# Kernel tuning notes

Measured on AMD Instinct MI355X. Metric: run time of the kernel, lower is better.

The kernel has to match this reference:

```python
import jax, jax.numpy as jnp
import numpy as np

NUM_HEADS = 16
NUM_KV_HEADS = 4
HEAD_SIZE = 128
SCALE = 1.0 / np.sqrt(128.0).astype(np.float32)
NEG_INF = -1e30


def setup_inputs() -> dict:
    key = jax.random.key(0)
    kq, kk, kv = jax.random.split(key, 3)
    B, S = 2, 2048
    query = jax.random.normal(kq, (B, NUM_HEADS, S, HEAD_SIZE), dtype=jnp.float32)
    k = jax.random.normal(kk, (B, NUM_KV_HEADS, S, HEAD_SIZE), dtype=jnp.float32)
    v = jax.random.normal(kv, (B, NUM_KV_HEADS, S, HEAD_SIZE), dtype=jnp.float32)
    return {"query": query, "key": k, "value": v}


def _attn(query, key, value):
    # query: [B, H, S, D]; key/value: [B, Hkv, S, D]; GQA with group = H // Hkv
    B, H, S, D = query.shape
    Hkv = key.shape[1]
    G = H // Hkv
    q = query.reshape(B, Hkv, G, S, D)
    # scores: [B, Hkv, G, Sq, Sk]
    scores = jnp.einsum('bkgsd,bktd->bkgst', q, key) * jnp.float32(SCALE)
    causal = jnp.tril(jnp.ones((S, S), dtype=bool))  # [Sq, Sk]
    scores = jnp.where(causal, scores, jnp.float32(NEG_INF))
    probs = jax.nn.softmax(scores, axis=-1)
    out = jnp.einsum('bkgst,bktd->bkgsd', probs, value)  # [B, Hkv, G, S, D]
    out = out.reshape(B, H, S, D)
    # transpose(1,2).reshape -> [B, S, H*D]
    return out.transpose(0, 2, 1, 3).reshape(B, S, H * D)


def reference(query, key, value):
    return _attn(query, key, value)
```

## Files before the change

### kernel.cpp

```cpp
#include <hip/hip_runtime.h>


#define S_LEN 2048
#define DH    128
#define NH    16
#define NKVH  4
#define NB    2
#define TQ    128
#define TK    64
#define NQT   (S_LEN / TQ)
#define QSCALE 0.12752749610559243f

typedef __attribute__((ext_vector_type(8))) short short8;
typedef __attribute__((ext_vector_type(4))) float f32x4;

#if __has_builtin(__builtin_amdgcn_exp2f)
#define EX2(x) __builtin_amdgcn_exp2f(x)
#else
#define EX2(x) exp2f(x)
#endif

__device__ __forceinline__ unsigned pk2(float a, float b) {
    union { float f; unsigned u; } x, y; x.f = a; y.f = b;
    return ((x.u + 0x8000u) >> 16) | ((y.u + 0x8000u) & 0xffff0000u);
}
__device__ __forceinline__ void cp16(const void* g, void* lds) {
    __builtin_amdgcn_global_load_lds(
        (const __attribute__((address_space(1))) void*)g,
        (__attribute__((address_space(3))) void*)lds, 16, 0, 0);
}

__global__ __launch_bounds__(256, 4)
void prepack(const float* __restrict__ K, const float* __restrict__ V,
             unsigned short* __restrict__ Kb, unsigned short* __restrict__ Vt) {
    if (blockIdx.y == 0) {
        const long long flat = (long long)blockIdx.x * 2048 + threadIdx.x * 8;
        const int s = (int)(flat >> 7) & (S_LEN - 1);
        const int d0 = (int)flat & 127;
        const float* p = K + flat;
        float4 x = *(const float4*)p;
        float4 y = *(const float4*)(p + 4);
        const int cs = (d0 >> 3) ^ (s & 7);
        uint4 o;
        o.x = pk2(x.x, x.y); o.y = pk2(x.z, x.w);
        o.z = pk2(y.x, y.y); o.w = pk2(y.z, y.w);
        *(uint4*)(Kb + (flat & ~127LL) + cs * 8) = o;
    } else {
        const int x = blockIdx.x;
        const int bkvh = x >> 7, sblk = (x >> 2) & 31, q = x & 3;
        const int tid = threadIdx.x;
        __shared__ unsigned Lt[64][17];
        const float* base = V + (size_t)bkvh * S_LEN * DH + (size_t)sblk * 64 * DH + q * 32;
#pragma unroll
        for (int j = 0; j < 2; ++j) {
            const int e = tid + j * 256;
            const int s = e >> 3, c4 = e & 7;
            float4 v = *(const float4*)(base + (size_t)s * DH + c4 * 4);
            Lt[s][c4 * 2]     = pk2(v.x, v.y);
            Lt[s][c4 * 2 + 1] = pk2(v.z, v.w);
        }
        __syncthreads();
        const unsigned short* lt = (const unsigned short*)&Lt[0][0];
        const int d_loc = tid >> 3, pc = tid & 7;
        const int d = q * 32 + d_loc;
        const int c_log = pc ^ (d & 7);
        unsigned short vv[8];
#pragma unroll
        for (int j = 0; j < 8; ++j) {
            const int kp = c_log * 8 + j;
            const int kv = (kp & 3) * 16 + (kp >> 2);
            vv[j] = lt[kv * 34 + d_loc];
        }
        uint4 o;
        o.x = (unsigned)vv[0] | ((unsigned)vv[1] << 16);
        o.y = (unsigned)vv[2] | ((unsigned)vv[3] << 16);
        o.z = (unsigned)vv[4] | ((unsigned)vv[5] << 16);
        o.w = (unsigned)vv[6] | ((unsigned)vv[7] << 16);
        *(uint4*)(Vt + (size_t)bkvh * S_LEN * DH + (size_t)d * S_LEN + sblk * 64 + pc * 8) = o;
    }
}

__global__ __launch_bounds__(256, 2)
void attn_fwd(const float* __restrict__ Q,
              const unsigned short* __restrict__ Kb,
              const unsigned short* __restrict__ Vtg,
              float* __restrict__ O,
              float* __restrict__ Opart,
              float* __restrict__ Lpart) {
    const int n    = blockIdx.x;
    const int g    = n & 7;
    const int b    = g >> 2;
    const int kvh  = g & 3;
    const int kk   = n >> 3;
    const int h    = kvh * 4 + (kk & 3);
    const int pr   = kk >> 2;
    const int a    = pr & 7;
    const int role = pr >> 3;
    const int sid  = ((b * NH + h) << 3) + a;

    const int tid  = threadIdx.x;
    const int w    = tid >> 6;
    const int lane = tid & 63;
    const int quad = lane >> 4;
    const int l16  = lane & 15;
    const int swz  = l16 & 7;

    int qt0, kt00, nr0, qt1; bool two_seg;
    if (role == 0) { qt0 = a;      kt00 = 0;         nr0 = 2 * a + 2;
                     qt1 = 15 - a; two_seg = true; }
    else           { qt0 = 15 - a; kt00 = 15 - 2*a;  nr0 = 17;
                     qt1 = 0;      two_seg = false; }

    __shared__ alignas(16) unsigned short Kl[2][TK][DH];
    __shared__ alignas(16) unsigned short Vl[2][DH][TK];
    __shared__ alignas(16) unsigned short Pl[TQ][64];

    const unsigned short* kb = Kb  + ((size_t)b * NKVH + kvh) * (size_t)(S_LEN * DH);
    const unsigned short* vb = Vtg + ((size_t)b * NKVH + kvh) * (size_t)(S_LEN * DH);

    auto stage = [&](int nb_, int kt) {
        const char* ks = (const char*)(kb + (size_t)kt * TK * DH);
        char* kd = (char*)&Kl[nb_][0][0] + w * 4096;
#pragma unroll
        for (int i = 0; i < 4; ++i)
            cp16(ks + w * 4096 + i * 1024 + lane * 16, kd + i * 1024);
        const char* vs = (const char*)vb + (size_t)kt * (TK * 2);
        char* vd = (char*)&Vl[nb_][0][0] + w * 4096;
#pragma unroll
        for (int i = 0; i < 4; ++i) {
            const int row = w * 32 + i * 8 + (lane >> 3);
            cp16(vs + (size_t)row * (S_LEN * 2) + (lane & 7) * 16, vd + i * 1024);
        }
    };
    auto ktof = [&](int r) { return r < nr0 ? kt00 + r : r - nr0; };

    stage(0, ktof(0));

    int qt  = qt0;
    int wq0 = qt * TQ + w * 32;
    int ntw = 2 * qt + 1 + (w >> 1);

    short8 aq[2][4];
    auto loadQ = [&]() {
#pragma unroll
        for (int sub = 0; sub < 2; ++sub) {
            const float* qp = Q + (((size_t)b * NH + h) * S_LEN + wq0 + sub * 16 + l16) * DH;
#pragma unroll
            for (int dc = 0; dc < 4; ++dc) {
                float4 xx = *(const float4*)(qp + dc * 32 + quad * 8);
                float4 yy = *(const float4*)(qp + dc * 32 + quad * 8 + 4);
                union { unsigned u[4]; short8 s; } tq;
                tq.u[0] = pk2(xx.x * QSCALE, xx.y * QSCALE);
                tq.u[1] = pk2(xx.z * QSCALE, xx.w * QSCALE);
                tq.u[2] = pk2(yy.x * QSCALE, yy.y * QSCALE);
                tq.u[3] = pk2(yy.z * QSCALE, yy.w * QSCALE);
                aq[sub][dc] = tq.s;
            }
        }
    };
    loadQ();

    f32x4 o[2][8];
    float lsum[2][4];
#pragma unroll
    for (int sub = 0; sub < 2; ++sub) {
#pragma unroll
        for (int ch = 0; ch < 8; ++ch) o[sub][ch] = (f32x4){0.f, 0.f, 0.f, 0.f};
#pragma unroll
        for (int r = 0; r < 4; ++r) lsum[sub][r] = 0.f;
    }

    __syncthreads();

    int cur = 0;
    for (int r = 0; r < 17; ++r) {
        if (r + 1 < 17) stage(cur ^ 1, ktof(r + 1));
        const int kt = ktof(r);
        if (kt < ntw) {
            const int j0 = kt * TK;
            const bool diag = (kt == ntw - 1);
            f32x4 s[2][4];
#pragma unroll
            for (int sub = 0; sub < 2; ++sub)
#pragma unroll
                for (int k4 = 0; k4 < 4; ++k4) s[sub][k4] = (f32x4){0.f, 0.f, 0.f, 0.f};
#pragma unroll
            for (int dc = 0; dc < 4; ++dc) {
#pragma unroll
                for (int k4 = 0; k4 < 4; ++k4) {
                    short8 bk = *(const short8*)&Kl[cur][k4 * 16 + l16][((dc * 4 + quad) ^ swz) * 8];
                    s[0][k4] = __builtin_amdgcn_mfma_f32_16x16x32_bf16(aq[0][dc], bk, s[0][k4], 0, 0, 0);
                    s[1][k4] = __builtin_amdgcn_mfma_f32_16x16x32_bf16(aq[1][dc], bk, s[1][k4], 0, 0, 0);
                }
            }
#pragma unroll
            for (int sub = 0; sub < 2; ++sub) {
                const int rb = wq0 + sub * 16 + quad * 4;
#pragma unroll
                for (int rr = 0; rr < 4; ++rr) {
                    float v0 = s[sub][0][rr], v1 = s[sub][1][rr];
                    float v2 = s[sub][2][rr], v3 = s[sub][3][rr];
                    if (diag) {
                        const int row = rb + rr;
                        if (j0 + l16      > row) v0 = -1e30f;
                        if (j0 + 16 + l16 > row) v1 = -1e30f;
                        if (j0 + 32 + l16 > row) v2 = -1e30f;
                        if (j0 + 48 + l16 > row) v3 = -1e30f;
                    }
                    float p0 = EX2(v0), p1 = EX2(v1), p2 = EX2(v2), p3 = EX2(v3);
                    lsum[sub][rr] += (p0 + p1) + (p2 + p3);
                    const int prow = w * 32 + sub * 16 + quad * 4 + rr;
                    const int wcol = (l16 * 8) ^ ((prow & 7) << 4);
                    *(uint2*)((char*)&Pl[0][0] + prow * 128 + wcol) =
                        make_uint2(pk2(p0, p1), pk2(p2, p3));
                }
            }
            const int rx = (l16 & 7) << 4;
#pragma unroll
            for (int kc = 0; kc < 2; ++kc) {
                const int cb = kc * 64 + quad * 16;
                short8 ap0 = *(const short8*)((const char*)&Pl[0][0] + (w * 32 + l16) * 128 + (cb ^ rx));
                short8 ap1 = *(const short8*)((const char*)&Pl[0][0] + (w * 32 + 16 + l16) * 128 + (cb ^ rx));
#pragma unroll
                for (int ch = 0; ch < 8; ++ch) {
                    short8 bv = *(const short8*)&Vl[cur][ch * 16 + l16][((kc * 4 + quad) ^ swz) * 8];
                    o[0][ch] = __builtin_amdgcn_mfma_f32_16x16x32_bf16(ap0, bv, o[0][ch], 0, 0, 0);
                    o[1][ch] = __builtin_amdgcn_mfma_f32_16x16x32_bf16(ap1, bv, o[1][ch], 0, 0, 0);
                }
            }
        }
        __syncthreads();
        cur ^= 1;
        if (two_seg && r == nr0 - 1) {
#pragma unroll
            for (int sub = 0; sub < 2; ++sub) {
#pragma unroll
                for (int rr = 0; rr < 4; ++rr) {
                    float rs = lsum[sub][rr];
                    rs += __shfl_xor(rs, 1);
                    rs += __shfl_xor(rs, 2);
                    rs += __shfl_xor(rs, 4);
                    rs += __shfl_xor(rs, 8);
                    const float invl = 1.f / rs;
                    const int row = wq0 + sub * 16 + quad * 4 + rr;
                    float* op = O + ((size_t)b * S_LEN + row) * (NH * DH) + h * DH;
#pragma unroll
                    for (int ch = 0; ch < 8; ++ch)
                        op[ch * 16 + l16] = o[sub][ch][rr] * invl;
                }
            }
            qt = qt1; wq0 = qt * TQ + w * 32; ntw = 2 * qt + 1 + (w >> 1);
            loadQ();
#pragma unroll
            for (int sub = 0; sub < 2; ++sub) {
#pragma unroll
                for (int ch = 0; ch < 8; ++ch) o[sub][ch] = (f32x4){0.f, 0.f, 0.f, 0.f};
#pragma unroll
                for (int rr = 0; rr < 4; ++rr) lsum[sub][rr] = 0.f;
            }
        }
    }

    float* lb = Lpart + (size_t)(role * 256 + sid) * 128;
#pragma unroll
    for (int sub = 0; sub < 2; ++sub) {
#pragma unroll
        for (int rr = 0; rr < 4; ++rr) {
            float rs = lsum[sub][rr];
            rs += __shfl_xor(rs, 1);
            rs += __shfl_xor(rs, 2);
            rs += __shfl_xor(rs, 4);
            rs += __shfl_xor(rs, 8);
            const int rl = w * 32 + sub * 16 + quad * 4 + rr;
            if (l16 == 0) lb[rl] = rs;
            float* op;
            if (role == 0) {
                const int row = wq0 + sub * 16 + quad * 4 + rr;
                op = O + ((size_t)b * S_LEN + row) * (NH * DH) + h * DH;
            } else {
                op = Opart + (size_t)sid * (128 * 128) + (size_t)rl * 128;
            }
#pragma unroll
            for (int ch = 0; ch < 8; ++ch)
                op[ch * 16 + l16] = o[sub][ch][rr];
        }
    }
}

__global__ __launch_bounds__(256)
void combine(const float* __restrict__ Opart, const float* __restrict__ Lpart,
             float* __restrict__ O) {
    const int blk = blockIdx.x;
    const int sid = blk >> 2;
    const int qp  = blk & 3;
    const int bh = sid >> 3, a = sid & 7;
    const int b = bh >> 4, h = bh & 15;
    const int qt = 15 - a;
    const float* o1 = Opart + (size_t)sid * (128 * 128);
    const float* l0 = Lpart + (size_t)sid * 128;
    const float* l1 = Lpart + (size_t)(256 + sid) * 128;
    const int tid = threadIdx.x;
#pragma unroll
    for (int i = 0; i < 4; ++i) {
        const int idx = qp * 1024 + i * 256 + tid;
        const int row = idx >> 5;
        const int c4  = idx & 31;
        const float inv = 1.f / (l0[row] + l1[row]);
        float* op = O + ((size_t)b * S_LEN + qt * 128 + row) * (NH * DH) + h * DH + c4 * 4;
        const float4 x = *(const float4*)op;
        const float4 y = ((const float4*)o1)[idx];
        float4 z;
        z.x = (x.x + y.x) * inv; z.y = (x.y + y.y) * inv;
        z.z = (x.z + y.z) * inv; z.w = (x.w + y.w) * inv;
        *(float4*)op = z;
    }
}

extern "C" void kernel_launch(void* const* d_in, const int* in_sizes, int n_in,
                              void* d_out, int out_size, void* d_ws, size_t ws_size,
                              hipStream_t stream) {
    const float* Q = (const float*)d_in[0];
    const float* K = (const float*)d_in[1];
    const float* V = (const float*)d_in[2];
    float* O = (float*)d_out;
    unsigned short* Kb = (unsigned short*)d_ws;
    unsigned short* Vt = Kb + (size_t)NB * NKVH * S_LEN * DH;
    float* Opart = (float*)(Vt + (size_t)NB * NKVH * S_LEN * DH);
    float* Lpart = Opart + (size_t)256 * 128 * 128;
    dim3 pgrid(NB * NKVH * (S_LEN / 16), 2);
    prepack<<<pgrid, 256, 0, stream>>>(K, V, Kb, Vt);
    attn_fwd<<<dim3(512), 256, 0, stream>>>(Q, Kb, Vt, O, Opart, Lpart);
    combine<<<dim3(1024), 256, 0, stream>>>(Opart, Lpart, O);
}
```

Measured before the change: 149.6 us.

## Compute S transposed so P feeds PV MFMA from registers, dropping LDS round-trip

Swaps the MFMA operands for QK^T so each lane holds scores for one query row across keys. The probabilities can then be packed straight into bf16 A-operands for the PV MFMA, with no write to and read back from a shared P tile. The V-transpose preprocessing permutes the key order to match this register layout. This also cuts the row-sum reduction to two cross-quad shuffles. In exchange it relies on the permuted V layout matching the MFMA lane mapping exactly, and uses a broadcast shuffle to fetch each row sum.

Measured after the change: 146.1 us. 1.02x faster.

```diff
diff --git a/kernel.cpp b/kernel.cpp
--- a/kernel.cpp
+++ b/kernel.cpp
@@ -68,7 +68,8 @@
 #pragma unroll
         for (int j = 0; j < 8; ++j) {
             const int kp = c_log * 8 + j;
-            const int kv = (kp & 3) * 16 + (kp >> 2);
+            const int kv = ((kp >> 5) & 1) * 32 + ((kp >> 2) & 1) * 16
+                         + ((kp >> 3) & 3) * 4 + (kp & 3);
             vv[j] = lt[kv * 34 + d_loc];
         }
         uint4 o;
@@ -113,19 +114,18 @@
 
     __shared__ alignas(16) unsigned short Kl[2][TK][DH];
     __shared__ alignas(16) unsigned short Vl[2][DH][TK];
-    __shared__ alignas(16) unsigned short Pl[TQ][64];
 
     const unsigned short* kb = Kb  + ((size_t)b * NKVH + kvh) * (size_t)(S_LEN * DH);
     const unsigned short* vb = Vtg + ((size_t)b * NKVH + kvh) * (size_t)(S_LEN * DH);
 
-    auto stage = [&](int nb_, int kt) {
+    auto stage = [&](int buf, int kt) {
         const char* ks = (const char*)(kb + (size_t)kt * TK * DH);
-        char* kd = (char*)&Kl[nb_][0][0] + w * 4096;
+        char* kd = (char*)&Kl[buf][0][0] + w * 4096;
 #pragma unroll
         for (int i = 0; i < 4; ++i)
             cp16(ks + w * 4096 + i * 1024 + lane * 16, kd + i * 1024);
         const char* vs = (const char*)vb + (size_t)kt * (TK * 2);
-        char* vd = (char*)&Vl[nb_][0][0] + w * 4096;
+        char* vd = (char*)&Vl[buf][0][0] + w * 4096;
 #pragma unroll
         for (int i = 0; i < 4; ++i) {
             const int row = w * 32 + i * 8 + (lane >> 3);
@@ -136,9 +136,12 @@
 
     stage(0, ktof(0));
 
-    int qt  = qt0;
-    int wq0 = qt * TQ + w * 32;
-    int ntw = 2 * qt + 1 + (w >> 1);
+    int qt, wq0, ntw;
+    auto setseg = [&](int q) {
+        qt = q; wq0 = qt * TQ + w * 32;
+        ntw = 2 * qt + 1 + (w >> 1);
+    };
+    setseg(qt0);
 
     short8 aq[2][4];
     auto loadQ = [&]() {
@@ -161,14 +164,11 @@
     loadQ();
 
     f32x4 o[2][8];
-    float lsum[2][4];
-#pragma unroll
-    for (int sub = 0; sub < 2; ++sub) {
+    float lsum[2] = {0.f, 0.f};
+#pragma unroll
+    for (int sub = 0; sub < 2; ++sub)
 #pragma unroll
         for (int ch = 0; ch < 8; ++ch) o[sub][ch] = (f32x4){0.f, 0.f, 0.f, 0.f};
-#pragma unroll
-        for (int r = 0; r < 4; ++r) lsum[sub][r] = 0.f;
-    }
 
     __syncthreads();
 
@@ -189,44 +189,43 @@
 #pragma unroll
                 for (int k4 = 0; k4 < 4; ++k4) {
                     short8 bk = *(const short8*)&Kl[cur][k4 * 16 + l16][((dc * 4 + quad) ^ swz) * 8];
-                    s[0][k4] = __builtin_amdgcn_mfma_f32_16x16x32_bf16(aq[0][dc], bk, s[0][k4], 0, 0, 0);
-                    s[1][k4] = __builtin_amdgcn_mfma_f32_16x16x32_bf16(aq[1][dc], bk, s[1][k4], 0, 0, 0);
+                    s[0][k4] = __builtin_amdgcn_mfma_f32_16x16x32_bf16(bk, aq[0][dc], s[0][k4], 0, 0, 0);
+                    s[1][k4] = __builtin_amdgcn_mfma_f32_16x16x32_bf16(bk, aq[1][dc], s[1][k4], 0, 0, 0);
                 }
             }
+            union { unsigned u[4]; short8 s8; } pa[2][2];
 #pragma unroll
             for (int sub = 0; sub < 2; ++sub) {
-                const int rb = wq0 + sub * 16 + quad * 4;
-#pragma unroll
-                for (int rr = 0; rr < 4; ++rr) {
-                    float v0 = s[sub][0][rr], v1 = s[sub][1][rr];
-                    float v2 = s[sub][2][rr], v3 = s[sub][3][rr];
-                    if (diag) {
-                        const int row = rb + rr;
-                        if (j0 + l16      > row) v0 = -1e30f;
-                        if (j0 + 16 + l16 > row) v1 = -1e30f;
-                        if (j0 + 32 + l16 > row) v2 = -1e30f;
-                        if (j0 + 48 + l16 > row) v3 = -1e30f;
+                const int qrow = wq0 + sub * 16 + l16;
+                float p[4][4];
+#pragma unroll
+                for (int k4 = 0; k4 < 4; ++k4) {
+#pragma unroll
+                    for (int rr = 0; rr < 4; ++rr) {
+                        float v = s[sub][k4][rr];
+                        if (diag && (j0 + k4 * 16 + quad * 4 + rr > qrow)) v = -1e30f;
+                        const float pe = EX2(v);
+                        lsum[sub] += pe;
+                        p[k4][rr] = pe;
                     }
-                    float p0 = EX2(v0), p1 = EX2(v1), p2 = EX2(v2), p3 = EX2(v3);
-                    lsum[sub][rr] += (p0 + p1) + (p2 + p3);
-                    const int prow = w * 32 + sub * 16 + quad * 4 + rr;
-                    const int wcol = (l16 * 8) ^ ((prow & 7) << 4);
-                    *(uint2*)((char*)&Pl[0][0] + prow * 128 + wcol) =
-                        make_uint2(pk2(p0, p1), pk2(p2, p3));
                 }
-            }
-            const int rx = (l16 & 7) << 4;
-#pragma unroll
-            for (int kc = 0; kc < 2; ++kc) {
-                const int cb = kc * 64 + quad * 16;
-                short8 ap0 = *(const short8*)((const char*)&Pl[0][0] + (w * 32 + l16) * 128 + (cb ^ rx));
-                short8 ap1 = *(const short8*)((const char*)&Pl[0][0] + (w * 32 + 16 + l16) * 128 + (cb ^ rx));
-#pragma unroll
-                for (int ch = 0; ch < 8; ++ch) {
-                    short8 bv = *(const short8*)&Vl[cur][ch * 16 + l16][((kc * 4 + quad) ^ swz) * 8];
-                    o[0][ch] = __builtin_amdgcn_mfma_f32_16x16x32_bf16(ap0, bv, o[0][ch], 0, 0, 0);
-                    o[1][ch] = __builtin_amdgcn_mfma_f32_16x16x32_bf16(ap1, bv, o[1][ch], 0, 0, 0);
-                }
+                pa[sub][0].u[0] = pk2(p[0][0], p[0][1]);
+                pa[sub][0].u[1] = pk2(p[0][2], p[0][3]);
+                pa[sub][0].u[2] = pk2(p[1][0], p[1][1]);
+                pa[sub][0].u[3] = pk2(p[1][2], p[1][3]);
+                pa[sub][1].u[0] = pk2(p[2][0], p[2][1]);
+                pa[sub][1].u[1] = pk2(p[2][2], p[2][3]);
+                pa[sub][1].u[2] = pk2(p[3][0], p[3][1]);
+                pa[sub][1].u[3] = pk2(p[3][2], p[3][3]);
+            }
+#pragma unroll
+            for (int ch = 0; ch < 8; ++ch) {
+                short8 bv0 = *(const short8*)&Vl[cur][ch * 16 + l16][(quad ^ swz) * 8];
+                o[0][ch] = __builtin_amdgcn_mfma_f32_16x16x32_bf16(pa[0][0].s8, bv0, o[0][ch], 0, 0, 0);
+                o[1][ch] = __builtin_amdgcn_mfma_f32_16x16x32_bf16(pa[1][0].s8, bv0, o[1][ch], 0, 0, 0);
+                short8 bv1 = *(const short8*)&Vl[cur][ch * 16 + l16][((4 + quad) ^ swz) * 8];
+                o[0][ch] = __builtin_amdgcn_mfma_f32_16x16x32_bf16(pa[0][1].s8, bv1, o[0][ch], 0, 0, 0);
+                o[1][ch] = __builtin_amdgcn_mfma_f32_16x16x32_bf16(pa[1][1].s8, bv1, o[1][ch], 0, 0, 0);
             }
         }
         __syncthreads();
@@ -234,14 +233,12 @@
         if (two_seg && r == nr0 - 1) {
 #pragma unroll
             for (int sub = 0; sub < 2; ++sub) {
+                float rs = lsum[sub];
+                rs += __shfl_xor(rs, 16);
+                rs += __shfl_xor(rs, 32);
 #pragma unroll
                 for (int rr = 0; rr < 4; ++rr) {
-                    float rs = lsum[sub][rr];
-                    rs += __shfl_xor(rs, 1);
-                    rs += __shfl_xor(rs, 2);
-                    rs += __shfl_xor(rs, 4);
-                    rs += __shfl_xor(rs, 8);
-                    const float invl = 1.f / rs;
+                    const float invl = 1.f / __shfl(rs, quad * 4 + rr);
                     const int row = wq0 + sub * 16 + quad * 4 + rr;
                     float* op = O + ((size_t)b * S_LEN + row) * (NH * DH) + h * DH;
 #pragma unroll
@@ -249,40 +246,38 @@
                         op[ch * 16 + l16] = o[sub][ch][rr] * invl;
                 }
             }
-            qt = qt1; wq0 = qt * TQ + w * 32; ntw = 2 * qt + 1 + (w >> 1);
+            setseg(qt1);
             loadQ();
 #pragma unroll
-            for (int sub = 0; sub < 2; ++sub) {
+            for (int sub = 0; sub < 2; ++sub)
 #pragma unroll
                 for (int ch = 0; ch < 8; ++ch) o[sub][ch] = (f32x4){0.f, 0.f, 0.f, 0.f};
-#pragma unroll
-                for (int rr = 0; rr < 4; ++rr) lsum[sub][rr] = 0.f;
-            }
+            lsum[0] = 0.f; lsum[1] = 0.f;
         }
     }
 
-    float* lb = Lpart + (size_t)(role * 256 + sid) * 128;
-#pragma unroll
-    for (int sub = 0; sub < 2; ++sub) {
-#pragma unroll
-        for (int rr = 0; rr < 4; ++rr) {
-            float rs = lsum[sub][rr];
-            rs += __shfl_xor(rs, 1);
-            rs += __shfl_xor(rs, 2);
-            rs += __shfl_xor(rs, 4);
-            rs += __shfl_xor(rs, 8);
-            const int rl = w * 32 + sub * 16 + quad * 4 + rr;
-            if (l16 == 0) lb[rl] = rs;
-            float* op;
-            if (role == 0) {
-                const int row = wq0 + sub * 16 + quad * 4 + rr;
-                op = O + ((size_t)b * S_LEN + row) * (NH * DH) + h * DH;
-            } else {
-                op = Opart + (size_t)sid * (128 * 128) + (size_t)rl * 128;
-            }
-#pragma unroll
-            for (int ch = 0; ch < 8; ++ch)
-                op[ch * 16 + l16] = o[sub][ch][rr];
+    {
+        float* lb = Lpart + (size_t)(role * 256 + sid) * 128;
+#pragma unroll
+        for (int sub = 0; sub < 2; ++sub) {
+            float rs = lsum[sub];
+            rs += __shfl_xor(rs, 16);
+            rs += __shfl_xor(rs, 32);
+            if (lane < 16) lb[w * 32 + sub * 16 + l16] = rs;
+#pragma unroll
+            for (int rr = 0; rr < 4; ++rr) {
+                const int rl = w * 32 + sub * 16 + quad * 4 + rr;
+                float* op;
+                if (role == 0) {
+                    const int row = wq0 + sub * 16 + quad * 4 + rr;
+                    op = O + ((size_t)b * S_LEN + row) * (NH * DH) + h * DH;
+                } else {
+                    op = Opart + (size_t)sid * (128 * 128) + (size_t)rl * 128;
+                }
+#pragma unroll
+                for (int ch = 0; ch < 8; ++ch)
+                    op[ch * 16 + l16] = o[sub][ch][rr];
+            }
         }
     }
 }
```
